# Kernel tuning notes

Measured on AMD Instinct MI355X. Metric: run time of the kernel, lower is better.

## Reference

```python
import jax, jax.numpy as jnp
import numpy as np

N = 50000        # nodes
E = 800000       # edges (avg degree 16)
C_IN = 64        # input_channels
H = 64           # hidden_channels
SLOPE = 0.01     # F.leaky_relu default negative_slope


def setup_inputs() -> dict:
    key = jax.random.key(0)
    ks = jax.random.split(key, 12)
    inp = {}
    inp["x"] = jax.random.normal(ks[0], (N, C_IN), dtype=jnp.float32)
    inp["edge_index"] = jax.random.randint(ks[1], (2, E), 0, N, dtype=jnp.int32)
    # SAGEConv params: lin_l (neighbors, with bias), lin_r (root, no bias)
    dims = [(C_IN, H), (H, H), (H, H)]
    for i, (ci, co) in enumerate(dims, start=1):
        s = 1.0 / np.sqrt(ci)
        inp[f"W_l{i}"] = jax.random.uniform(ks[2 * i], (ci, co), jnp.float32, -s, s)
        inp[f"b_l{i}"] = jnp.zeros((co,), jnp.float32)
        inp[f"W_r{i}"] = jax.random.uniform(ks[2 * i + 1], (ci, co), jnp.float32, -s, s)
    s = 1.0 / np.sqrt(H)
    inp["W_out"] = jax.random.uniform(ks[8], (H, 1), jnp.float32, -s, s)
    inp["b_out"] = jnp.zeros((1,), jnp.float32)
    return inp


def reference(x, edge_index, W_l1, b_l1, W_r1, W_l2, b_l2, W_r2,
              W_l3, b_l3, W_r3, W_out, b_out):
    src, dst = edge_index[0], edge_index[1]
    # per-destination degree for mean aggregation (isolated nodes -> 0)
    deg = jax.ops.segment_sum(jnp.ones((src.shape[0],), x.dtype), dst,
                              num_segments=N)
    inv_deg = (1.0 / jnp.maximum(deg, 1.0))[:, None]  # [N,1]

    def sage(h, Wl, bl, Wr):
        # gather source features, mean-reduce onto destinations
        mean_nb = jax.ops.segment_sum(h[src], dst, num_segments=N) * inv_deg
        out = mean_nb @ Wl + bl + h @ Wr
        # dropout is identity in eval mode
        return jax.nn.leaky_relu(out, SLOPE)

    h = sage(x, W_l1, b_l1, W_r1)
    h = sage(h, W_l2, b_l2, W_r2)
    h = sage(h, W_l3, b_l3, W_r3)
    return (h @ W_out + b_out).squeeze()  # [N]
```

## Files before the change

### kernel.cpp

```cpp
#include <hip/hip_runtime.h>

#define HD 64
#define SLOPE 0.01f
#define BSH 6
#define BNODES 64
#define CHUNK 4096
#define SLOT 1536


__global__ __launch_bounds__(256) void part_kernel(const int* __restrict__ ei,
                                                   int* __restrict__ bcur,
                                                   int* __restrict__ ebuf,
                                                   int E, int nb) {
    __shared__ int pk_s[CHUNK];
    __shared__ int mt_s[CHUNK];
    __shared__ int hist[784];
    __shared__ int sbase[784];
    const int t = threadIdx.x;
    const int c0 = blockIdx.x * CHUNK;
    const int cnt = min(CHUNK, E - c0);
    for (int i = t; i < nb; i += 256) hist[i] = 0;
    __syncthreads();
    for (int i = t; i < cnt; i += 256) {
        int src = ei[c0 + i];
        int dst = ei[E + c0 + i];
        int b = dst >> BSH;
        pk_s[i] = (src << BSH) | (dst & (BNODES - 1));
        int r = atomicAdd(&hist[b], 1);
        mt_s[i] = (b << 12) | r;
    }
    __syncthreads();
    for (int b = t; b < nb; b += 256) {
        int h = hist[b];
        if (h) sbase[b] = b * SLOT + atomicAdd(&bcur[b], h);
    }
    __syncthreads();
    for (int i = t; i < cnt; i += 256) {
        int m = mt_s[i];
        int b = m >> 12;
        ebuf[sbase[b] + (m & (CHUNK - 1))] = pk_s[i];
    }
}

__global__ __launch_bounds__(256) void bsort_kernel(const int* __restrict__ ebuf,
                                                    const int* __restrict__ bcnt,
                                                    int* __restrict__ colidx,
                                                    int* __restrict__ rowptr,
                                                    int* __restrict__ rowend,
                                                    float* __restrict__ invdeg,
                                                    const float* __restrict__ x,
                                                    _Float16* __restrict__ h16a,
                                                    int n, int n64) {
    __shared__ int cnt[BNODES];
    const int b = blockIdx.x;
    const int t = threadIdx.x;
    const int ebeg = b * SLOT;
    const int eend = ebeg + bcnt[b];
    if (t < BNODES) cnt[t] = 0;
    __syncthreads();
    for (int k = ebeg + t; k < eend; k += 256)
        atomicAdd(&cnt[ebuf[k] & (BNODES - 1)], 1);
    __syncthreads();
    if (t < BNODES) {
        int v = cnt[t];
        int x2 = v;
        #pragma unroll
        for (int d = 1; d < 64; d <<= 1) { int y = __shfl_up(x2, d, 64); if (t >= d) x2 += y; }
        int excl = x2 - v;
        int node = b * BNODES + t;
        if (node < n) {
            rowptr[node] = ebeg + excl;
            rowend[node] = ebeg + excl + v;
            invdeg[node] = 1.0f / (float)((v > 1) ? v : 1);
        }
        cnt[t] = excl;
    }
    __syncthreads();
    for (int k = ebeg + t; k < eend; k += 256) {
        int p = ebuf[k];
        int r = atomicAdd(&cnt[p & (BNODES - 1)], 1);
        colidx[ebeg + r] = p >> BSH;
    }
    const int total8 = n64 >> 3;
    for (int i = b * 256 + t; i < total8; i += gridDim.x * 256) {
        int e = i * 8;
        float4 a = *(const float4*)(x + e);
        float4 c = *(const float4*)(x + e + 4);
        _Float16 o[8] = {(_Float16)a.x, (_Float16)a.y, (_Float16)a.z, (_Float16)a.w,
                         (_Float16)c.x, (_Float16)c.y, (_Float16)c.z, (_Float16)c.w};
        *(float4*)(h16a + e) = *(float4*)o;
    }
}


#define FMA4(acc, am, b0, b1, b2, b3)                                  \
    acc.x += am.x * b0.x + am.y * b1.x + am.z * b2.x + am.w * b3.x;    \
    acc.y += am.x * b0.y + am.y * b1.y + am.z * b2.y + am.w * b3.y;    \
    acc.z += am.x * b0.z + am.y * b1.z + am.z * b2.z + am.w * b3.z;    \
    acc.w += am.x * b0.w + am.y * b1.w + am.z * b2.w + am.w * b3.w;

#define FUSED_BODY(EXTRA_SHARED)                                            \
    __shared__ float sA[64 * 68];            \
    __shared__ float sS[64 * 68];                       \
    EXTRA_SHARED                                                            \
    const int t = threadIdx.x;                                              \
    const int lane = t & 63;                                                \
    const int w = t >> 6;                                                   \
    const int base = blockIdx.x * 64;                                       \
    const int rows = min(64, n - base);                                     \
    const float4* __restrict__ g4 = (const float4*)h16_in;                  \
        \
    _Pragma("unroll")                                                       \
    for (int idx = 0; idx < 2; ++idx) {                                     \
        int i = t + idx * 256;                                  \
        int r = i >> 3, cc = i & 7;                                         \
        float4 raw = {0.f, 0.f, 0.f, 0.f};                                  \
        if (r < rows) raw = g4[(size_t)(base + r) * 8 + cc];                \
        const _Float16* hp = (const _Float16*)&raw;                         \
        float4 lo = {(float)hp[0], (float)hp[1], (float)hp[2], (float)hp[3]}; \
        float4 hi = {(float)hp[4], (float)hp[5], (float)hp[6], (float)hp[7]}; \
        *(float4*)(sS + r * 68 + cc * 8 + 0) = lo;                          \
        *(float4*)(sS + r * 68 + cc * 8 + 4) = hi;                          \
    }                                                                       \
                                  \
    {                                                                       \
        const int g = lane >> 3;                        \
        const int c8 = lane & 7;            \
        _Pragma("unroll")                                                   \
        for (int pass = 0; pass < 2; ++pass) {                              \
            const int r = w * 16 + pass * 8 + g;       \
            const int node = base + r;                                      \
            const bool valid = node < n;                                    \
            int beg = 0, end = 0; float idg = 0.f;                          \
            if (valid) {                                                    \
                beg = rowptr[node];                                         \
                end = rowend[node];                                         \
                idg = invdeg[node];                                         \
            }                                                               \
            const int deg = end - beg;                                      \
            int md = deg;                             \
            md = max(md, __shfl_xor(md, 8, 64));                            \
            md = max(md, __shfl_xor(md, 16, 64));                           \
            md = max(md, __shfl_xor(md, 32, 64));                           \
            float4 accA = {0.f, 0.f, 0.f, 0.f};                             \
            float4 accB = {0.f, 0.f, 0.f, 0.f};                             \
            for (int t0 = 0; t0 < md; t0 += 8) {                            \
                const int off = beg + t0 + c8;                              \
                int ci = (off < end) ? colidx[off] : 0;                     \
                int idx[8];                                                 \
                _Pragma("unroll")                                           \
                for (int k = 0; k < 8; ++k)                                 \
                    idx[k] = __shfl(ci, g * 8 + k, 64);                     \
                float4 vv[8];                                               \
                float sel[8];                                               \
                _Pragma("unroll")                                           \
                for (int k = 0; k < 8; ++k) {                               \
                    const bool p = (t0 + k) < deg;                          \
                    const int safe = p ? idx[k] : 0;                        \
                    sel[k] = p ? 1.0f : 0.0f;                               \
                    vv[k] = g4[(size_t)safe * 8 + c8];                      \
                }                                                           \
                _Pragma("unroll")                                           \
                for (int k = 0; k < 8; ++k) {                               \
                    const _Float16* hp = (const _Float16*)&vv[k];           \
                    accA.x += sel[k] * (float)hp[0];                        \
                    accA.y += sel[k] * (float)hp[1];                        \
                    accA.z += sel[k] * (float)hp[2];                        \
                    accA.w += sel[k] * (float)hp[3];                        \
                    accB.x += sel[k] * (float)hp[4];                        \
                    accB.y += sel[k] * (float)hp[5];                        \
                    accB.z += sel[k] * (float)hp[6];                        \
                    accB.w += sel[k] * (float)hp[7];                        \
                }                                                           \
            }                                                               \
            float4 oA = {accA.x * idg, accA.y * idg, accA.z * idg, accA.w * idg}; \
            float4 oB = {accB.x * idg, accB.y * idg, accB.z * idg, accB.w * idg}; \
            *(float4*)(sA + r * 68 + c8 * 8 + 0) = oA;                      \
            *(float4*)(sA + r * 68 + c8 * 8 + 4) = oB;                      \
        }                                                                   \
    }                                                                       \
    __syncthreads();                                                        \
      \
    const int r0 = t & 15;                                                  \
    const int jq = t >> 4;                                        \
    const int j0 = jq * 4;                                                  \
    const float4* __restrict__ Wl4 = (const float4*)Wl;                     \
    const float4* __restrict__ Wr4 = (const float4*)Wr;                     \
    const float4 bias = *(const float4*)(bl + j0);                          \
    float4 acc0 = bias, acc1 = bias, acc2 = bias, acc3 = bias;              \
    _Pragma("unroll 2")                                                     \
    for (int k4 = 0; k4 < 16; ++k4) {                                       \
        float4 b0 = Wl4[(4 * k4 + 0) * 16 + jq];                            \
        float4 b1 = Wl4[(4 * k4 + 1) * 16 + jq];                            \
        float4 b2 = Wl4[(4 * k4 + 2) * 16 + jq];                            \
        float4 b3 = Wl4[(4 * k4 + 3) * 16 + jq];                            \
        float4 a0 = *(const float4*)(sA + (r0 +  0) * 68 + 4 * k4);         \
        float4 a1 = *(const float4*)(sA + (r0 + 16) * 68 + 4 * k4);         \
        float4 a2 = *(const float4*)(sA + (r0 + 32) * 68 + 4 * k4);         \
        float4 a3 = *(const float4*)(sA + (r0 + 48) * 68 + 4 * k4);         \
        FMA4(acc0, a0, b0, b1, b2, b3)                                      \
        FMA4(acc1, a1, b0, b1, b2, b3)                                      \
        FMA4(acc2, a2, b0, b1, b2, b3)                                      \
        FMA4(acc3, a3, b0, b1, b2, b3)                                      \
        b0 = Wr4[(4 * k4 + 0) * 16 + jq];                                   \
        b1 = Wr4[(4 * k4 + 1) * 16 + jq];                                   \
        b2 = Wr4[(4 * k4 + 2) * 16 + jq];                                   \
        b3 = Wr4[(4 * k4 + 3) * 16 + jq];                                   \
        a0 = *(const float4*)(sS + (r0 +  0) * 68 + 4 * k4);                \
        a1 = *(const float4*)(sS + (r0 + 16) * 68 + 4 * k4);                \
        a2 = *(const float4*)(sS + (r0 + 32) * 68 + 4 * k4);                \
        a3 = *(const float4*)(sS + (r0 + 48) * 68 + 4 * k4);                \
        FMA4(acc0, a0, b0, b1, b2, b3)                                      \
        FMA4(acc1, a1, b0, b1, b2, b3)                                      \
        FMA4(acc2, a2, b0, b1, b2, b3)                                      \
        FMA4(acc3, a3, b0, b1, b2, b3)                                      \
    }                                                                       \
    acc0.x = (acc0.x > 0.f) ? acc0.x : SLOPE * acc0.x;                      \
    acc0.y = (acc0.y > 0.f) ? acc0.y : SLOPE * acc0.y;                      \
    acc0.z = (acc0.z > 0.f) ? acc0.z : SLOPE * acc0.z;                      \
    acc0.w = (acc0.w > 0.f) ? acc0.w : SLOPE * acc0.w;                      \
    acc1.x = (acc1.x > 0.f) ? acc1.x : SLOPE * acc1.x;                      \
    acc1.y = (acc1.y > 0.f) ? acc1.y : SLOPE * acc1.y;                      \
    acc1.z = (acc1.z > 0.f) ? acc1.z : SLOPE * acc1.z;                      \
    acc1.w = (acc1.w > 0.f) ? acc1.w : SLOPE * acc1.w;                      \
    acc2.x = (acc2.x > 0.f) ? acc2.x : SLOPE * acc2.x;                      \
    acc2.y = (acc2.y > 0.f) ? acc2.y : SLOPE * acc2.y;                      \
    acc2.z = (acc2.z > 0.f) ? acc2.z : SLOPE * acc2.z;                      \
    acc2.w = (acc2.w > 0.f) ? acc2.w : SLOPE * acc2.w;                      \
    acc3.x = (acc3.x > 0.f) ? acc3.x : SLOPE * acc3.x;                      \
    acc3.y = (acc3.y > 0.f) ? acc3.y : SLOPE * acc3.y;                      \
    acc3.z = (acc3.z > 0.f) ? acc3.z : SLOPE * acc3.z;                      \
    acc3.w = (acc3.w > 0.f) ? acc3.w : SLOPE * acc3.w;

__global__ __launch_bounds__(256, 4) void sage_fused(
    const _Float16* __restrict__ h16_in, _Float16* __restrict__ h16_out,
    const int* __restrict__ rowptr, const int* __restrict__ rowend,
    const int* __restrict__ colidx, const float* __restrict__ invdeg,
    const float* __restrict__ Wl, const float* __restrict__ bl,
    const float* __restrict__ Wr, int n) {
    FUSED_BODY()
    #define STORE_ROW(S, ACC)                                               \
        { int r = r0 + 16 * S;                                              \
          if (r < rows) {                                                   \
              _Float16 o[4] = {(_Float16)ACC.x, (_Float16)ACC.y,            \
                               (_Float16)ACC.z, (_Float16)ACC.w};           \
              *(float2*)(h16_out + (size_t)(base + r) * HD + j0)            \
                  = *(float2*)o;                                            \
          } }
    STORE_ROW(0, acc0)
    STORE_ROW(1, acc1)
    STORE_ROW(2, acc2)
    STORE_ROW(3, acc3)
    #undef STORE_ROW
}

__global__ __launch_bounds__(256, 4) void sage_fused_out(
    const _Float16* __restrict__ h16_in,
    const int* __restrict__ rowptr, const int* __restrict__ rowend,
    const int* __restrict__ colidx, const float* __restrict__ invdeg,
    const float* __restrict__ Wl, const float* __restrict__ bl,
    const float* __restrict__ Wr,
    const float* __restrict__ Wout, const float* __restrict__ bout,
    float* __restrict__ out, int n) {
    FUSED_BODY(__shared__ float s_part[16][64];)
    const float4 w4 = *(const float4*)(Wout + j0);
    s_part[jq][r0 +  0] = acc0.x * w4.x + acc0.y * w4.y + acc0.z * w4.z + acc0.w * w4.w;
    s_part[jq][r0 + 16] = acc1.x * w4.x + acc1.y * w4.y + acc1.z * w4.z + acc1.w * w4.w;
    s_part[jq][r0 + 32] = acc2.x * w4.x + acc2.y * w4.y + acc2.z * w4.z + acc2.w * w4.w;
    s_part[jq][r0 + 48] = acc3.x * w4.x + acc3.y * w4.y + acc3.z * w4.z + acc3.w * w4.w;
    __syncthreads();
    if (t < 64) {
        float sum = 0.f;
        #pragma unroll
        for (int g2 = 0; g2 < 16; ++g2) sum += s_part[g2][t];
        if (t < rows) out[base + t] = sum + bout[0];
    }
}


extern "C" void kernel_launch(void* const* d_in, const int* in_sizes, int n_in,
                              void* d_out, int out_size, void* d_ws, size_t ws_size,
                              hipStream_t stream) {
    const float* x   = (const float*)d_in[0];
    const int* ei    = (const int*)d_in[1];
    const float* Wl1 = (const float*)d_in[2];
    const float* bl1 = (const float*)d_in[3];
    const float* Wr1 = (const float*)d_in[4];
    const float* Wl2 = (const float*)d_in[5];
    const float* bl2 = (const float*)d_in[6];
    const float* Wr2 = (const float*)d_in[7];
    const float* Wl3 = (const float*)d_in[8];
    const float* bl3 = (const float*)d_in[9];
    const float* Wr3 = (const float*)d_in[10];
    const float* Wout = (const float*)d_in[11];
    const float* bout = (const float*)d_in[12];
    float* out = (float*)d_out;

    const int N = in_sizes[0] / HD;
    const int E = in_sizes[1] / 2;
    const int NB = (N + BNODES - 1) >> BSH;
    const int n64 = N * HD;

    _Float16* h16a = (_Float16*)d_ws;
    _Float16* h16b = h16a + (size_t)N * HD;
    int* ebuf     = (int*)(h16b + (size_t)N * HD);
    int* colidx   = ebuf + (size_t)NB * SLOT;
    int* rowptr   = colidx + (size_t)NB * SLOT;
    int* rowend   = rowptr + N;
    float* invdeg = (float*)(rowend + N);
    int* bcur     = (int*)(invdeg + N);

    hipMemsetAsync(bcur, 0, 784 * sizeof(int), stream);

    part_kernel<<<(E + CHUNK - 1) / CHUNK, 256, 0, stream>>>(ei, bcur, ebuf, E, NB);
    bsort_kernel<<<NB, 256, 0, stream>>>(ebuf, bcur, colidx, rowptr, rowend,
                                         invdeg, x, h16a, N, n64);

    const int ggrid = (N + 63) / 64;

    sage_fused<<<ggrid, 256, 0, stream>>>(h16a, h16b,
                                          rowptr, rowend, colidx, invdeg,
                                          Wl1, bl1, Wr1, N);
    sage_fused<<<ggrid, 256, 0, stream>>>(h16b, h16a,
                                          rowptr, rowend, colidx, invdeg,
                                          Wl2, bl2, Wr2, N);
    sage_fused_out<<<ggrid, 256, 0, stream>>>(h16a,
                                              rowptr, rowend, colidx, invdeg,
                                              Wl3, bl3, Wr3, Wout, bout, out, N);
}
```

Measured before the change: 205.3 us.

## Replace two-pass bucketed CSR build with fixed-capacity padded adjacency lists

Drops the partition and bucket-sort kernels. A single build kernel now appends each edge's source straight into a per-node slot of MAXDEG=64 entries, using a global atomic counter per destination, and computes inverse degree on the fly inside the SAGE kernels. This removes one kernel launch, the intermediate edge buffer and the rowptr/rowend/invdeg arrays. In exchange it relies on no node having more than 64 incoming edges: an overflowing node would drop edges, and the gather would read into the next node's slots. It also adds contended global atomics and scattered writes across a larger padded array.

```diff
diff --git a/kernel.cpp b/kernel.cpp
--- a/kernel.cpp
+++ b/kernel.cpp
@@ -2,87 +2,26 @@
 
 #define HD 64
 #define SLOPE 0.01f
-#define BSH 6
-#define BNODES 64
-#define CHUNK 4096
-#define SLOT 1536
-
-
-__global__ __launch_bounds__(256) void part_kernel(const int* __restrict__ ei,
-                                                   int* __restrict__ bcur,
-                                                   int* __restrict__ ebuf,
-                                                   int E, int nb) {
-    __shared__ int pk_s[CHUNK];
-    __shared__ int mt_s[CHUNK];
-    __shared__ int hist[784];
-    __shared__ int sbase[784];
-    const int t = threadIdx.x;
-    const int c0 = blockIdx.x * CHUNK;
-    const int cnt = min(CHUNK, E - c0);
-    for (int i = t; i < nb; i += 256) hist[i] = 0;
-    __syncthreads();
-    for (int i = t; i < cnt; i += 256) {
-        int src = ei[c0 + i];
-        int dst = ei[E + c0 + i];
-        int b = dst >> BSH;
-        pk_s[i] = (src << BSH) | (dst & (BNODES - 1));
-        int r = atomicAdd(&hist[b], 1);
-        mt_s[i] = (b << 12) | r;
-    }
-    __syncthreads();
-    for (int b = t; b < nb; b += 256) {
-        int h = hist[b];
-        if (h) sbase[b] = b * SLOT + atomicAdd(&bcur[b], h);
-    }
-    __syncthreads();
-    for (int i = t; i < cnt; i += 256) {
-        int m = mt_s[i];
-        int b = m >> 12;
-        ebuf[sbase[b] + (m & (CHUNK - 1))] = pk_s[i];
-    }
-}
-
-__global__ __launch_bounds__(256) void bsort_kernel(const int* __restrict__ ebuf,
-                                                    const int* __restrict__ bcnt,
+#define MAXDEG 64
+#define MDSH 6
+
+
+__global__ __launch_bounds__(256) void build_kernel(const int* __restrict__ ei,
+                                                    int* __restrict__ degv,
                                                     int* __restrict__ colidx,
-                                                    int* __restrict__ rowptr,
-                                                    int* __restrict__ rowend,
-                                                    float* __restrict__ invdeg,
                                                     const float* __restrict__ x,
                                                     _Float16* __restrict__ h16a,
-                                                    int n, int n64) {
-    __shared__ int cnt[BNODES];
-    const int b = blockIdx.x;
-    const int t = threadIdx.x;
-    const int ebeg = b * SLOT;
-    const int eend = ebeg + bcnt[b];
-    if (t < BNODES) cnt[t] = 0;
-    __syncthreads();
-    for (int k = ebeg + t; k < eend; k += 256)
-        atomicAdd(&cnt[ebuf[k] & (BNODES - 1)], 1);
-    __syncthreads();
-    if (t < BNODES) {
-        int v = cnt[t];
-        int x2 = v;
-        #pragma unroll
-        for (int d = 1; d < 64; d <<= 1) { int y = __shfl_up(x2, d, 64); if (t >= d) x2 += y; }
-        int excl = x2 - v;
-        int node = b * BNODES + t;
-        if (node < n) {
-            rowptr[node] = ebeg + excl;
-            rowend[node] = ebeg + excl + v;
-            invdeg[node] = 1.0f / (float)((v > 1) ? v : 1);
-        }
-        cnt[t] = excl;
-    }
-    __syncthreads();
-    for (int k = ebeg + t; k < eend; k += 256) {
-        int p = ebuf[k];
-        int r = atomicAdd(&cnt[p & (BNODES - 1)], 1);
-        colidx[ebeg + r] = p >> BSH;
+                                                    int E, int n64) {
+    const int tid = blockIdx.x * 256 + threadIdx.x;
+    const int stride = gridDim.x * 256;
+    for (int i = tid; i < E; i += stride) {
+        int src = ei[i];
+        int dst = ei[E + i];
+        int r = atomicAdd(&degv[dst], 1);
+        if (r < MAXDEG) colidx[(dst << MDSH) + r] = src;
     }
     const int total8 = n64 >> 3;
-    for (int i = b * 256 + t; i < total8; i += gridDim.x * 256) {
+    for (int i = tid; i < total8; i += stride) {
         int e = i * 8;
         float4 a = *(const float4*)(x + e);
         float4 c = *(const float4*)(x + e + 4);
@@ -131,13 +70,11 @@
             const int r = w * 16 + pass * 8 + g;       \
             const int node = base + r;                                      \
             const bool valid = node < n;                                    \
-            int beg = 0, end = 0; float idg = 0.f;                          \
-            if (valid) {                                                    \
-                beg = rowptr[node];                                         \
-                end = rowend[node];                                         \
-                idg = invdeg[node];                                         \
-            }                                                               \
-            const int deg = end - beg;                                      \
+            int deg = 0;                                                    \
+            if (valid) deg = degv[node];                                    \
+            const int beg = node << MDSH;                                   \
+            const int end = beg + deg;                                      \
+            const float idg = 1.0f / (float)((deg > 1) ? deg : 1);          \
             int md = deg;                             \
             md = max(md, __shfl_xor(md, 8, 64));                            \
             md = max(md, __shfl_xor(md, 16, 64));                           \
@@ -234,8 +171,7 @@
 
 __global__ __launch_bounds__(256, 4) void sage_fused(
     const _Float16* __restrict__ h16_in, _Float16* __restrict__ h16_out,
-    const int* __restrict__ rowptr, const int* __restrict__ rowend,
-    const int* __restrict__ colidx, const float* __restrict__ invdeg,
+    const int* __restrict__ colidx, const int* __restrict__ degv,
     const float* __restrict__ Wl, const float* __restrict__ bl,
     const float* __restrict__ Wr, int n) {
     FUSED_BODY()
@@ -256,8 +192,7 @@
 
 __global__ __launch_bounds__(256, 4) void sage_fused_out(
     const _Float16* __restrict__ h16_in,
-    const int* __restrict__ rowptr, const int* __restrict__ rowend,
-    const int* __restrict__ colidx, const float* __restrict__ invdeg,
+    const int* __restrict__ colidx, const int* __restrict__ degv,
     const float* __restrict__ Wl, const float* __restrict__ bl,
     const float* __restrict__ Wr,
     const float* __restrict__ Wout, const float* __restrict__ bout,
@@ -298,33 +233,23 @@
 
     const int N = in_sizes[0] / HD;
     const int E = in_sizes[1] / 2;
-    const int NB = (N + BNODES - 1) >> BSH;
     const int n64 = N * HD;
 
     _Float16* h16a = (_Float16*)d_ws;
     _Float16* h16b = h16a + (size_t)N * HD;
-    int* ebuf     = (int*)(h16b + (size_t)N * HD);
-    int* colidx   = ebuf + (size_t)NB * SLOT;
-    int* rowptr   = colidx + (size_t)NB * SLOT;
-    int* rowend   = rowptr + N;
-    float* invdeg = (float*)(rowend + N);
-    int* bcur     = (int*)(invdeg + N);
-
-    hipMemsetAsync(bcur, 0, 784 * sizeof(int), stream);
-
-    part_kernel<<<(E + CHUNK - 1) / CHUNK, 256, 0, stream>>>(ei, bcur, ebuf, E, NB);
-    bsort_kernel<<<NB, 256, 0, stream>>>(ebuf, bcur, colidx, rowptr, rowend,
-                                         invdeg, x, h16a, N, n64);
+    int* colidx   = (int*)(h16b + (size_t)N * HD);
+    int* degv     = colidx + (size_t)N * MAXDEG;
+
+    hipMemsetAsync(degv, 0, (size_t)N * sizeof(int), stream);
+
+    build_kernel<<<2048, 256, 0, stream>>>(ei, degv, colidx, x, h16a, E, n64);
 
     const int ggrid = (N + 63) / 64;
 
-    sage_fused<<<ggrid, 256, 0, stream>>>(h16a, h16b,
-                                          rowptr, rowend, colidx, invdeg,
+    sage_fused<<<ggrid, 256, 0, stream>>>(h16a, h16b, colidx, degv,
                                           Wl1, bl1, Wr1, N);
-    sage_fused<<<ggrid, 256, 0, stream>>>(h16b, h16a,
-                                          rowptr, rowend, colidx, invdeg,
+    sage_fused<<<ggrid, 256, 0, stream>>>(h16b, h16a, colidx, degv,
                                           Wl2, bl2, Wr2, N);
-    sage_fused_out<<<ggrid, 256, 0, stream>>>(h16a,
-                                              rowptr, rowend, colidx, invdeg,
+    sage_fused_out<<<ggrid, 256, 0, stream>>>(h16a, colidx, degv,
                                               Wl3, bl3, Wr3, Wout, bout, out, N);
 }
```

Measured after the change: 242.7 us. 18.2% more time.

## Halve node tile to 32 and prefetch column indices in gather loop

Applied to the files above, without the earlier changes.

Shrinks each fused SAGE block from 64 to 32 destination nodes, so each 8-lane group handles a single node rather than two passes. The grid doubles and launch bounds rise to allow 6 blocks per CU. The neighbor loop now runs to each group's own degree instead of the wave-wide maximum, and it prefetches the next batch of column indices while the current batch is being gathered. The aim is better latency hiding and occupancy for the irregular gather, at the cost of reading each weight tile twice as often across the grid and reusing fewer weights per block in the small GEMM.

```diff
diff --git a/kernel.cpp b/kernel.cpp
--- a/kernel.cpp
+++ b/kernel.cpp
@@ -6,6 +6,7 @@
 #define BNODES 64
 #define CHUNK 4096
 #define SLOT 1536
+#define TN 32
 
 
 __global__ __launch_bounds__(256) void part_kernel(const int* __restrict__ ei,
@@ -100,20 +101,18 @@
     acc.w += am.x * b0.w + am.y * b1.w + am.z * b2.w + am.w * b3.w;
 
 #define FUSED_BODY(EXTRA_SHARED)                                            \
-    __shared__ float sA[64 * 68];            \
-    __shared__ float sS[64 * 68];                       \
+    __shared__ float sA[TN * 68];            \
+    __shared__ float sS[TN * 68];                       \
     EXTRA_SHARED                                                            \
     const int t = threadIdx.x;                                              \
     const int lane = t & 63;                                                \
     const int w = t >> 6;                                                   \
-    const int base = blockIdx.x * 64;                                       \
-    const int rows = min(64, n - base);                                     \
+    const int base = blockIdx.x * TN;                                       \
+    const int rows = min(TN, n - base);                                     \
     const float4* __restrict__ g4 = (const float4*)h16_in;                  \
         \
-    _Pragma("unroll")                                                       \
-    for (int idx = 0; idx < 2; ++idx) {                                     \
-        int i = t + idx * 256;                                  \
-        int r = i >> 3, cc = i & 7;                                         \
+    {                                                                       \
+        int r = t >> 3, cc = t & 7;           \
         float4 raw = {0.f, 0.f, 0.f, 0.f};                                  \
         if (r < rows) raw = g4[(size_t)(base + r) * 8 + cc];                \
         const _Float16* hp = (const _Float16*)&raw;                         \
@@ -122,72 +121,70 @@
         *(float4*)(sS + r * 68 + cc * 8 + 0) = lo;                          \
         *(float4*)(sS + r * 68 + cc * 8 + 4) = hi;                          \
     }                                                                       \
-                                  \
+       \
     {                                                                       \
         const int g = lane >> 3;                        \
         const int c8 = lane & 7;            \
-        _Pragma("unroll")                                                   \
-        for (int pass = 0; pass < 2; ++pass) {                              \
-            const int r = w * 16 + pass * 8 + g;       \
-            const int node = base + r;                                      \
-            const bool valid = node < n;                                    \
-            int beg = 0, end = 0; float idg = 0.f;                          \
-            if (valid) {                                                    \
-                beg = rowptr[node];                                         \
-                end = rowend[node];                                         \
-                idg = invdeg[node];                                         \
+        const int r = w * 8 + g;                       \
+        const int node = base + r;                                          \
+        const bool valid = node < n;                                        \
+        int beg = 0, end = 0; float idg = 0.f;                              \
+        if (valid) {                                                        \
+            beg = rowptr[node];                                             \
+            end = rowend[node];                                             \
+            idg = invdeg[node];                                             \
+        }                                                                   \
+        const int deg = end - beg;                                          \
+        float4 accA = {0.f, 0.f, 0.f, 0.f};                                 \
+        float4 accB = {0.f, 0.f, 0.f, 0.f};                                 \
+        int off0 = beg + c8;                                                \
+        int ci = (off0 < end) ? colidx[off0] : 0;                           \
+        for (int t0 = 0; t0 < deg; t0 += 8) {          \
+            const int ci_cur = ci;                                          \
+            {                          \
+                int offn = beg + t0 + 8 + c8;                               \
+                ci = (offn < end) ? colidx[offn] : 0;                       \
             }                                                               \
-            const int deg = end - beg;                                      \
-            int md = deg;                             \
-            md = max(md, __shfl_xor(md, 8, 64));                            \
-            md = max(md, __shfl_xor(md, 16, 64));                           \
-            md = max(md, __shfl_xor(md, 32, 64));                           \
-            float4 accA = {0.f, 0.f, 0.f, 0.f};                             \
-            float4 accB = {0.f, 0.f, 0.f, 0.f};                             \
-            for (int t0 = 0; t0 < md; t0 += 8) {                            \
-                const int off = beg + t0 + c8;                              \
-                int ci = (off < end) ? colidx[off] : 0;                     \
-                int idx[8];                                                 \
-                _Pragma("unroll")                                           \
-                for (int k = 0; k < 8; ++k)                                 \
-                    idx[k] = __shfl(ci, g * 8 + k, 64);                     \
-                float4 vv[8];                                               \
-                float sel[8];                                               \
-                _Pragma("unroll")                                           \
-                for (int k = 0; k < 8; ++k) {                               \
-                    const bool p = (t0 + k) < deg;                          \
-                    const int safe = p ? idx[k] : 0;                        \
-                    sel[k] = p ? 1.0f : 0.0f;                               \
-                    vv[k] = g4[(size_t)safe * 8 + c8];                      \
-                }                                                           \
-                _Pragma("unroll")                                           \
-                for (int k = 0; k < 8; ++k) {                               \
-                    const _Float16* hp = (const _Float16*)&vv[k];           \
-                    accA.x += sel[k] * (float)hp[0];                        \
-                    accA.y += sel[k] * (float)hp[1];                        \
-                    accA.z += sel[k] * (float)hp[2];                        \
-                    accA.w += sel[k] * (float)hp[3];                        \
-                    accB.x += sel[k] * (float)hp[4];                        \
-                    accB.y += sel[k] * (float)hp[5];                        \
-                    accB.z += sel[k] * (float)hp[6];                        \
-                    accB.w += sel[k] * (float)hp[7];                        \
-                }                                                           \
+            int idx[8];                                                     \
+            _Pragma("unroll")                                               \
+            for (int k = 0; k < 8; ++k)                                     \
+                idx[k] = __shfl(ci_cur, g * 8 + k, 64);                     \
+            float4 vv[8];                                                   \
+            float sel[8];                                                   \
+            _Pragma("unroll")                                               \
+            for (int k = 0; k < 8; ++k) {                                   \
+                const bool p = (t0 + k) < deg;                              \
+                const int safe = p ? idx[k] : 0;                            \
+                sel[k] = p ? 1.0f : 0.0f;                                   \
+                vv[k] = g4[(size_t)safe * 8 + c8];                          \
             }                                                               \
-            float4 oA = {accA.x * idg, accA.y * idg, accA.z * idg, accA.w * idg}; \
-            float4 oB = {accB.x * idg, accB.y * idg, accB.z * idg, accB.w * idg}; \
-            *(float4*)(sA + r * 68 + c8 * 8 + 0) = oA;                      \
-            *(float4*)(sA + r * 68 + c8 * 8 + 4) = oB;                      \
+            _Pragma("unroll")                                               \
+            for (int k = 0; k < 8; ++k) {                                   \
+                const _Float16* hp = (const _Float16*)&vv[k];               \
+                accA.x += sel[k] * (float)hp[0];                            \
+                accA.y += sel[k] * (float)hp[1];                            \
+                accA.z += sel[k] * (float)hp[2];                            \
+                accA.w += sel[k] * (float)hp[3];                            \
+                accB.x += sel[k] * (float)hp[4];                            \
+                accB.y += sel[k] * (float)hp[5];                            \
+                accB.z += sel[k] * (float)hp[6];                            \
+                accB.w += sel[k] * (float)hp[7];                            \
+            }                                                               \
         }                                                                   \
+        float4 oA = {accA.x * idg, accA.y * idg, accA.z * idg, accA.w * idg}; \
+        float4 oB = {accB.x * idg, accB.y * idg, accB.z * idg, accB.w * idg}; \
+        *(float4*)(sA + r * 68 + c8 * 8 + 0) = oA;                          \
+        *(float4*)(sA + r * 68 + c8 * 8 + 4) = oB;                          \
     }                                                                       \
     __syncthreads();                                                        \
-      \
+         \
     const int r0 = t & 15;                                                  \
     const int jq = t >> 4;                                        \
     const int j0 = jq * 4;                                                  \
     const float4* __restrict__ Wl4 = (const float4*)Wl;                     \
     const float4* __restrict__ Wr4 = (const float4*)Wr;                     \
     const float4 bias = *(const float4*)(bl + j0);                          \
-    float4 acc0 = bias, acc1 = bias, acc2 = bias, acc3 = bias;              \
+    float4 acc0 = bias, acc1 = bias;                                        \
     _Pragma("unroll 2")                                                     \
     for (int k4 = 0; k4 < 16; ++k4) {                                       \
         float4 b0 = Wl4[(4 * k4 + 0) * 16 + jq];                            \
@@ -196,24 +193,16 @@
         float4 b3 = Wl4[(4 * k4 + 3) * 16 + jq];                            \
         float4 a0 = *(const float4*)(sA + (r0 +  0) * 68 + 4 * k4);         \
         float4 a1 = *(const float4*)(sA + (r0 + 16) * 68 + 4 * k4);         \
-        float4 a2 = *(const float4*)(sA + (r0 + 32) * 68 + 4 * k4);         \
-        float4 a3 = *(const float4*)(sA + (r0 + 48) * 68 + 4 * k4);         \
         FMA4(acc0, a0, b0, b1, b2, b3)                                      \
         FMA4(acc1, a1, b0, b1, b2, b3)                                      \
-        FMA4(acc2, a2, b0, b1, b2, b3)                                      \
-        FMA4(acc3, a3, b0, b1, b2, b3)                                      \
         b0 = Wr4[(4 * k4 + 0) * 16 + jq];                                   \
         b1 = Wr4[(4 * k4 + 1) * 16 + jq];                                   \
         b2 = Wr4[(4 * k4 + 2) * 16 + jq];                                   \
         b3 = Wr4[(4 * k4 + 3) * 16 + jq];                                   \
         a0 = *(const float4*)(sS + (r0 +  0) * 68 + 4 * k4);                \
         a1 = *(const float4*)(sS + (r0 + 16) * 68 + 4 * k4);                \
-        a2 = *(const float4*)(sS + (r0 + 32) * 68 + 4 * k4);                \
-        a3 = *(const float4*)(sS + (r0 + 48) * 68 + 4 * k4);                \
         FMA4(acc0, a0, b0, b1, b2, b3)                                      \
         FMA4(acc1, a1, b0, b1, b2, b3)                                      \
-        FMA4(acc2, a2, b0, b1, b2, b3)                                      \
-        FMA4(acc3, a3, b0, b1, b2, b3)                                      \
     }                                                                       \
     acc0.x = (acc0.x > 0.f) ? acc0.x : SLOPE * acc0.x;                      \
     acc0.y = (acc0.y > 0.f) ? acc0.y : SLOPE * acc0.y;                      \
@@ -222,17 +211,9 @@
     acc1.x = (acc1.x > 0.f) ? acc1.x : SLOPE * acc1.x;                      \
     acc1.y = (acc1.y > 0.f) ? acc1.y : SLOPE * acc1.y;                      \
     acc1.z = (acc1.z > 0.f) ? acc1.z : SLOPE * acc1.z;                      \
-    acc1.w = (acc1.w > 0.f) ? acc1.w : SLOPE * acc1.w;                      \
-    acc2.x = (acc2.x > 0.f) ? acc2.x : SLOPE * acc2.x;                      \
-    acc2.y = (acc2.y > 0.f) ? acc2.y : SLOPE * acc2.y;                      \
-    acc2.z = (acc2.z > 0.f) ? acc2.z : SLOPE * acc2.z;                      \
-    acc2.w = (acc2.w > 0.f) ? acc2.w : SLOPE * acc2.w;                      \
-    acc3.x = (acc3.x > 0.f) ? acc3.x : SLOPE * acc3.x;                      \
-    acc3.y = (acc3.y > 0.f) ? acc3.y : SLOPE * acc3.y;                      \
-    acc3.z = (acc3.z > 0.f) ? acc3.z : SLOPE * acc3.z;                      \
-    acc3.w = (acc3.w > 0.f) ? acc3.w : SLOPE * acc3.w;
-
-__global__ __launch_bounds__(256, 4) void sage_fused(
+    acc1.w = (acc1.w > 0.f) ? acc1.w : SLOPE * acc1.w;
+
+__global__ __launch_bounds__(256, 6) void sage_fused(
     const _Float16* __restrict__ h16_in, _Float16* __restrict__ h16_out,
     const int* __restrict__ rowptr, const int* __restrict__ rowend,
     const int* __restrict__ colidx, const float* __restrict__ invdeg,
@@ -249,12 +230,10 @@
           } }
     STORE_ROW(0, acc0)
     STORE_ROW(1, acc1)
-    STORE_ROW(2, acc2)
-    STORE_ROW(3, acc3)
     #undef STORE_ROW
 }
 
-__global__ __launch_bounds__(256, 4) void sage_fused_out(
+__global__ __launch_bounds__(256, 6) void sage_fused_out(
     const _Float16* __restrict__ h16_in,
     const int* __restrict__ rowptr, const int* __restrict__ rowend,
     const int* __restrict__ colidx, const float* __restrict__ invdeg,
@@ -262,14 +241,12 @@
     const float* __restrict__ Wr,
     const float* __restrict__ Wout, const float* __restrict__ bout,
     float* __restrict__ out, int n) {
-    FUSED_BODY(__shared__ float s_part[16][64];)
+    FUSED_BODY(__shared__ float s_part[16][TN];)
     const float4 w4 = *(const float4*)(Wout + j0);
     s_part[jq][r0 +  0] = acc0.x * w4.x + acc0.y * w4.y + acc0.z * w4.z + acc0.w * w4.w;
     s_part[jq][r0 + 16] = acc1.x * w4.x + acc1.y * w4.y + acc1.z * w4.z + acc1.w * w4.w;
-    s_part[jq][r0 + 32] = acc2.x * w4.x + acc2.y * w4.y + acc2.z * w4.z + acc2.w * w4.w;
-    s_part[jq][r0 + 48] = acc3.x * w4.x + acc3.y * w4.y + acc3.z * w4.z + acc3.w * w4.w;
-    __syncthreads();
-    if (t < 64) {
+    __syncthreads();
+    if (t < TN) {
         float sum = 0.f;
         #pragma unroll
         for (int g2 = 0; g2 < 16; ++g2) sum += s_part[g2][t];
@@ -316,7 +293,7 @@
     bsort_kernel<<<NB, 256, 0, stream>>>(ebuf, bcur, colidx, rowptr, rowend,
                                          invdeg, x, h16a, N, n64);
 
-    const int ggrid = (N + 63) / 64;
+    const int ggrid = (N + TN - 1) / TN;
 
     sage_fused<<<ggrid, 256, 0, stream>>>(h16a, h16b,
                                           rowptr, rowend, colidx, invdeg,
```

New measurement: 256.4 us. 1.25x slower.
